# Kernel tuning notes

Measured on AMD Instinct MI355X. Metric: run time of the kernel, lower is better.

## Reference

```python
import jax, jax.numpy as jnp
import numpy as np

BATCH, SEQ, DIM = 2048, 200, 300


def setup_inputs() -> dict:
    key = jax.random.key(0)
    k_vec, k_keep = jax.random.split(key)
    word_vecs = jax.random.normal(k_vec, (BATCH, SEQ, DIM), dtype=jnp.float32)
    # original module's count_nonzero check). Force the first word of every
    # sentence to be kept so no sentence is empty (original would crash on
    # an empty stack anyway).
    keep = jax.random.bernoulli(k_keep, 0.5, (BATCH, SEQ))
    keep = keep.at[:, 0].set(True)
    word_vecs = word_vecs * keep[:, :, None].astype(jnp.float32)
    return {"word_vecs": word_vecs}


def reference(word_vecs):
    # mask[b, s] = True iff word vector has any nonzero component
    mask = jnp.any(word_vecs != 0, axis=-1)                      # [B, S]
    maskf = mask.astype(word_vecs.dtype)
    # masked sum over words, divided by count of kept words -> masked mean
    sums = jnp.einsum("bsd,bs->bd", word_vecs, maskf)            # [B, D]
    counts = jnp.sum(maskf, axis=-1, keepdims=True)              # [B, 1]
    return sums / counts
```

## Files before the change

### kernel.cpp

```cpp
#include <hip/hip_runtime.h>


#define SR_BATCH 2048
#define SR_SEQ   200
#define SR_DIM   300

__global__ __launch_bounds__(256) void sentence_rep_kernel(
    const float* __restrict__ in, float* __restrict__ out) {
    const int b    = blockIdx.x;
    const int lane = threadIdx.x & 63;
    const int wave = threadIdx.x >> 6;

    const float* base = in + (size_t)b * (SR_SEQ * SR_DIM);

    float a0x = 0.f, a0y = 0.f, a0z = 0.f, a0w = 0.f;
    float a1x = 0.f, a1y = 0.f, a1z = 0.f, a1w = 0.f;
    float cnt = 0.f;

    const bool has_tail = (lane < 11);

    for (int s = wave; s < SR_SEQ; s += 4) {
        const float4* row4 = (const float4*)(base + s * SR_DIM);
        float4 v0 = row4[lane];
        float4 v1 = make_float4(0.f, 0.f, 0.f, 0.f);
        if (has_tail) v1 = row4[64 + lane];

        bool nz = (v0.x != 0.f) | (v0.y != 0.f) | (v0.z != 0.f) | (v0.w != 0.f) |
                  (v1.x != 0.f) | (v1.y != 0.f) | (v1.z != 0.f) | (v1.w != 0.f);

        if (__ballot(nz) != 0ULL) {
            a0x += v0.x; a0y += v0.y; a0z += v0.z; a0w += v0.w;
            a1x += v1.x; a1y += v1.y; a1z += v1.z; a1w += v1.w;
            cnt += 1.f;
        }
    }

    __shared__ float s_acc[4][304];
    __shared__ float s_cnt[4];

    {
        float* dst = &s_acc[wave][0];
        const int d0 = lane * 4;
        dst[d0 + 0] = a0x; dst[d0 + 1] = a0y; dst[d0 + 2] = a0z; dst[d0 + 3] = a0w;
        if (has_tail) {
            const int d1 = 256 + lane * 4;
            dst[d1 + 0] = a1x; dst[d1 + 1] = a1y; dst[d1 + 2] = a1z; dst[d1 + 3] = a1w;
        }
        if (lane == 0) s_cnt[wave] = cnt;
    }
    __syncthreads();

    const float total = s_cnt[0] + s_cnt[1] + s_cnt[2] + s_cnt[3];
    float* orow = out + (size_t)b * SR_DIM;
    for (int d = threadIdx.x; d < SR_DIM; d += 256) {
        float sum = s_acc[0][d] + s_acc[1][d] + s_acc[2][d] + s_acc[3][d];
        orow[d] = sum / total;
    }
}

extern "C" void kernel_launch(void* const* d_in, const int* in_sizes, int n_in,
                              void* d_out, int out_size, void* d_ws, size_t ws_size,
                              hipStream_t stream) {
    const float* in = (const float*)d_in[0];
    float* out = (float*)d_out;
    sentence_rep_kernel<<<SR_BATCH, 256, 0, stream>>>(in, out);
}
```

Measured before the change: 87.93 us.

## Stream sentence as flat float4 array with LDS accumulation and row bitmask counting

Replaces the per-row wave loop, which left many lanes idle on the 75-float4 row tail, with a flat coalesced sweep over all float4s of a sentence. Each wave accumulates into its own LDS row by column. Zero rows are summed unconditionally, which is safe because masked rows are all zeros. Kept rows are counted by building per-row nonzero bitmasks, OR-reducing them across lanes and waves, and taking a popcount. This adds per-element LDS read-modify-write and integer division in exchange for full lane utilization on global loads.

Measured after the change: 93.41 us. +6.2%, slower.

```diff
diff --git a/kernel.cpp b/kernel.cpp
--- a/kernel.cpp
+++ b/kernel.cpp
@@ -1,60 +1,108 @@
 #include <hip/hip_runtime.h>
 
 
-#define SR_BATCH 2048
-#define SR_SEQ   200
-#define SR_DIM   300
+typedef float f4 __attribute__((ext_vector_type(4)));
+
+#define SR_BATCH     2048
+#define SR_SEQ       200
+#define SR_DIM       300
+#define F4_PER_ROW   75
+#define F4_PER_SENT  (SR_SEQ * F4_PER_ROW)
+#define NTHREADS     256
+#define NSWEEP_FULL  58
+#define TAIL_THREADS 152
 
 __global__ __launch_bounds__(256) void sentence_rep_kernel(
     const float* __restrict__ in, float* __restrict__ out) {
     const int b    = blockIdx.x;
-    const int lane = threadIdx.x & 63;
-    const int wave = threadIdx.x >> 6;
+    const int t    = threadIdx.x;
+    const int wave = t >> 6;
+    const int lane = t & 63;
 
-    const float* base = in + (size_t)b * (SR_SEQ * SR_DIM);
-
-    float a0x = 0.f, a0y = 0.f, a0z = 0.f, a0w = 0.f;
-    float a1x = 0.f, a1y = 0.f, a1z = 0.f, a1w = 0.f;
-    float cnt = 0.f;
-
-    const bool has_tail = (lane < 11);
-
-    for (int s = wave; s < SR_SEQ; s += 4) {
-        const float4* row4 = (const float4*)(base + s * SR_DIM);
-        float4 v0 = row4[lane];
-        float4 v1 = make_float4(0.f, 0.f, 0.f, 0.f);
-        if (has_tail) v1 = row4[64 + lane];
-
-        bool nz = (v0.x != 0.f) | (v0.y != 0.f) | (v0.z != 0.f) | (v0.w != 0.f) |
-                  (v1.x != 0.f) | (v1.y != 0.f) | (v1.z != 0.f) | (v1.w != 0.f);
-
-        if (__ballot(nz) != 0ULL) {
-            a0x += v0.x; a0y += v0.y; a0z += v0.z; a0w += v0.w;
-            a1x += v1.x; a1y += v1.y; a1z += v1.z; a1w += v1.w;
-            cnt += 1.f;
-        }
-    }
-
-    __shared__ float s_acc[4][304];
-    __shared__ float s_cnt[4];
+    __shared__ f4 s_acc[4][F4_PER_ROW];
+    __shared__ unsigned long long s_mask[4][4];
+    __shared__ float s_count;
 
     {
-        float* dst = &s_acc[wave][0];
-        const int d0 = lane * 4;
-        dst[d0 + 0] = a0x; dst[d0 + 1] = a0y; dst[d0 + 2] = a0z; dst[d0 + 3] = a0w;
-        if (has_tail) {
-            const int d1 = 256 + lane * 4;
-            dst[d1 + 0] = a1x; dst[d1 + 1] = a1y; dst[d1 + 2] = a1z; dst[d1 + 3] = a1w;
-        }
-        if (lane == 0) s_cnt[wave] = cnt;
+        f4* flat = &s_acc[0][0];
+        f4 z = {0.f, 0.f, 0.f, 0.f};
+        flat[t] = z;
+        if (t < 4 * F4_PER_ROW - NTHREADS) flat[NTHREADS + t] = z;
     }
     __syncthreads();
 
-    const float total = s_cnt[0] + s_cnt[1] + s_cnt[2] + s_cnt[3];
-    float* orow = out + (size_t)b * SR_DIM;
-    for (int d = threadIdx.x; d < SR_DIM; d += 256) {
-        float sum = s_acc[0][d] + s_acc[1][d] + s_acc[2][d] + s_acc[3][d];
-        orow[d] = sum / total;
+    const f4* __restrict__ src = (const f4*)(in + (size_t)b * (SR_SEQ * SR_DIM));
+    f4* myacc = &s_acc[wave][0];
+
+    unsigned long long m0 = 0, m1 = 0, m2 = 0, m3 = 0;
+
+    int f = t;
+    #pragma unroll 2
+    for (int k = 0; k < NSWEEP_FULL; ++k, f += NTHREADS) {
+        f4 v = src[f];
+        const int r = f / F4_PER_ROW;
+        const int c = f - r * F4_PER_ROW;
+
+        f4 a = myacc[c];
+        a.x += v.x; a.y += v.y; a.z += v.z; a.w += v.w;
+        myacc[c] = a;
+
+        const bool nz = (v.x != 0.f) | (v.y != 0.f) | (v.z != 0.f) | (v.w != 0.f);
+        const unsigned long long bit = nz ? (1ULL << (r & 63)) : 0ULL;
+        const int sel = r >> 6;
+        m0 |= (sel == 0) ? bit : 0ULL;
+        m1 |= (sel == 1) ? bit : 0ULL;
+        m2 |= (sel == 2) ? bit : 0ULL;
+        m3 |= (sel == 3) ? bit : 0ULL;
+    }
+    if (t < TAIL_THREADS) {
+        f4 v = src[f];
+        const int r = f / F4_PER_ROW;
+        const int c = f - r * F4_PER_ROW;
+
+        f4 a = myacc[c];
+        a.x += v.x; a.y += v.y; a.z += v.z; a.w += v.w;
+        myacc[c] = a;
+
+        const bool nz = (v.x != 0.f) | (v.y != 0.f) | (v.z != 0.f) | (v.w != 0.f);
+        const unsigned long long bit = nz ? (1ULL << (r & 63)) : 0ULL;
+        const int sel = r >> 6;
+        m0 |= (sel == 0) ? bit : 0ULL;
+        m1 |= (sel == 1) ? bit : 0ULL;
+        m2 |= (sel == 2) ? bit : 0ULL;
+        m3 |= (sel == 3) ? bit : 0ULL;
+    }
+
+    for (int off = 1; off < 64; off <<= 1) {
+        m0 |= __shfl_xor(m0, off, 64);
+        m1 |= __shfl_xor(m1, off, 64);
+        m2 |= __shfl_xor(m2, off, 64);
+        m3 |= __shfl_xor(m3, off, 64);
+    }
+    if (lane == 0) {
+        s_mask[wave][0] = m0; s_mask[wave][1] = m1;
+        s_mask[wave][2] = m2; s_mask[wave][3] = m3;
+    }
+    __syncthreads();
+
+    if (t == 0) {
+        unsigned long long r0 = s_mask[0][0] | s_mask[1][0] | s_mask[2][0] | s_mask[3][0];
+        unsigned long long r1 = s_mask[0][1] | s_mask[1][1] | s_mask[2][1] | s_mask[3][1];
+        unsigned long long r2 = s_mask[0][2] | s_mask[1][2] | s_mask[2][2] | s_mask[3][2];
+        unsigned long long r3 = s_mask[0][3] | s_mask[1][3] | s_mask[2][3] | s_mask[3][3];
+        s_count = (float)(__popcll(r0) + __popcll(r1) + __popcll(r2) + __popcll(r3));
+    }
+    __syncthreads();
+
+    if (t < F4_PER_ROW) {
+        const float total = s_count;
+        f4 o0 = s_acc[0][t], o1 = s_acc[1][t], o2 = s_acc[2][t], o3 = s_acc[3][t];
+        f4 o;
+        o.x = (o0.x + o1.x + o2.x + o3.x) / total;
+        o.y = (o0.y + o1.y + o2.y + o3.y) / total;
+        o.z = (o0.z + o1.z + o2.z + o3.z) / total;
+        o.w = (o0.w + o1.w + o2.w + o3.w) / total;
+        ((f4*)(out + (size_t)b * SR_DIM))[t] = o;
     }
 }
 
@@ -63,5 +111,5 @@
                               hipStream_t stream) {
     const float* in = (const float*)d_in[0];
     float* out = (float*)d_out;
-    sentence_rep_kernel<<<SR_BATCH, 256, 0, stream>>>(in, out);
+    sentence_rep_kernel<<<SR_BATCH, NTHREADS, 0, stream>>>(in, out);
 }
```
